# Kernel tuning notes

Measured on AMD Instinct MI355X. Metric: run time of the kernel, lower is better.

The kernel has to match this reference:

```python
import jax, jax.numpy as jnp
import numpy as np

EPS = 1.1920929e-07  # torch RMSNorm default eps = finfo(fp32).eps


def _rmsnorm(x, w):
    return x * jax.lax.rsqrt(jnp.mean(x * x, axis=-1, keepdims=True) + EPS) * w


def setup_inputs() -> dict:
    B, S, D, H, SD = 2, 2048, 1024, 16, 64
    ks = jax.random.split(jax.random.key(0), 16)
    scale = 0.02
    return {
        "x": jax.random.normal(ks[0], (B, S, D), jnp.float32),
        "gamma": jax.random.normal(ks[1], (1, 1, D), jnp.float32),
        "beta": jax.random.normal(ks[2], (1, 1, D), jnp.float32),
        "state": jax.random.normal(ks[3], (B, SD), jnp.float32),
        # weights stored as (in, out) so y = x @ W
        "w_qkv": jax.random.normal(ks[4], (D, 3 * D), jnp.float32) * scale,
        "w_o": jax.random.normal(ks[5], (D, D), jnp.float32) * scale,
        "w_gate": jax.random.normal(ks[6], (D, 3 * D), jnp.float32) * scale,
        "w_up": jax.random.normal(ks[7], (D, 3 * D), jnp.float32) * scale,
        "w_down": jax.random.normal(ks[8], (3 * D, D), jnp.float32) * scale,
        "norm1_w": jnp.ones((D,), jnp.float32),
        "norm2_w": jnp.ones((D,), jnp.float32),
        "w_state_mod": jax.random.normal(ks[9], (SD, 2 * D), jnp.float32) * scale,
        "w_h2s": jax.random.normal(ks[10], (D, SD), jnp.float32) * scale,
        "w_sgate": jax.random.normal(ks[11], (2 * SD, SD), jnp.float32) * scale,
    }


def reference(x, gamma, beta, state, w_qkv, w_o, w_gate, w_up, w_down,
              norm1_w, norm2_w, w_state_mod, w_h2s, w_sgate):
    B, S, D = x.shape
    H = 16
    hd = D // H

    # state-conditioned FiLM modulation
    state_mod = state @ w_state_mod                      # (B, 2D)
    state_gamma = 1.0 + state_mod[:, :D][:, None, :]     # (B, 1, D)
    state_beta = state_mod[:, D:][:, None, :]
    full_gamma = gamma * state_gamma
    full_beta = beta + state_beta

    # attention branch
    h = _rmsnorm(x, norm1_w) * full_gamma + full_beta
    qkv = (h @ w_qkv).reshape(B, S, 3, H, hd)
    q = qkv[:, :, 0].transpose(0, 2, 1, 3)               # (B, H, S, hd)
    k = qkv[:, :, 1].transpose(0, 2, 1, 3)
    v = qkv[:, :, 2].transpose(0, 2, 1, 3)
    scores = jnp.einsum('bhqd,bhkd->bhqk', q, k) / np.sqrt(hd).astype(np.float32)
    causal = jnp.tril(jnp.ones((S, S), bool))
    scores = jnp.where(causal, scores, -jnp.inf)
    attn = jax.nn.softmax(scores, axis=-1)
    out = jnp.einsum('bhqk,bhkd->bhqd', attn, v).transpose(0, 2, 1, 3).reshape(B, S, D)
    x = x + out @ w_o

    # SwiGLU FFN branch (same FiLM params)
    h2 = _rmsnorm(x, norm2_w) * full_gamma + full_beta
    gate = jax.nn.silu(h2 @ w_gate)
    x = x + (gate * (h2 @ w_up)) @ w_down

    # recurrent state update
    new_info = jnp.mean(x, axis=1) @ w_h2s               # (B, SD)
    update_gate = jax.nn.sigmoid(jnp.concatenate([state, new_info], axis=-1) @ w_sgate)
    new_state = state * (1.0 - update_gate) + new_info * update_gate
    return x, new_state
```

## Files before the change

kernel.cpp:

```cpp
#include <hip/hip_runtime.h>
#include <hip/hip_bf16.h>

#define EPS_RMS 1.1920929e-07f

constexpr int B_ = 2, S_ = 2048, D_ = 1024, H_ = 16, HD_ = 64, SD_ = 64;
constexpr int M_ = B_ * S_;
constexpr int D3_ = 3 * D_;

using short8 = __attribute__((ext_vector_type(8))) short;
using f32x4  = __attribute__((ext_vector_type(4))) float;
using f32x16 = __attribute__((ext_vector_type(16))) float;

static __device__ __forceinline__ ushort f2bf(float x) {
  __hip_bfloat16 h = __float2bfloat16(x);
  return *reinterpret_cast<ushort*>(&h);
}
static __device__ __forceinline__ float bf2f(ushort u) {
  __hip_bfloat16 h;
  *reinterpret_cast<ushort*>(&h) = u;
  return __bfloat162float(h);
}
static __device__ __forceinline__ unsigned pk2(float lo, float hi) {
  return (unsigned)f2bf(lo) | ((unsigned)f2bf(hi) << 16);
}
struct alignas(8) bf4 { ushort a, b, c, d; };

static __device__ __forceinline__ void gload16(const ushort* g, ushort* l) {
  __builtin_amdgcn_global_load_lds(
      (const __attribute__((address_space(1))) unsigned int*)g,
      (__attribute__((address_space(3))) unsigned int*)l, 16, 0, 0);
}

__global__ void film_kernel(const float* __restrict__ state,
                            const float* __restrict__ w_sm,
                            const float* __restrict__ gamma,
                            const float* __restrict__ beta,
                            float* __restrict__ fg, float* __restrict__ fb) {
  int c = blockIdx.x * 256 + threadIdx.x;
  int b = blockIdx.y;
  float acc = 0.f;
#pragma unroll 8
  for (int k = 0; k < SD_; ++k)
    acc += state[b * SD_ + k] * w_sm[k * (2 * D_) + c];
  if (c < D_) fg[b * D_ + c] = gamma[c] * (1.f + acc);
  else        fb[b * D_ + (c - D_)] = beta[c - D_] + acc;
}

__global__ __launch_bounds__(256) void rmsnorm_film_kernel(
    const float* __restrict__ X, const float* __restrict__ nw,
    const float* __restrict__ fg, const float* __restrict__ fb,
    ushort* __restrict__ Hout) {
  int row = blockIdx.x;
  int b = row / S_;
  int t = threadIdx.x;
  const float4* x4 = (const float4*)(X + (size_t)row * D_);
  float4 xv = x4[t];
  float ss = xv.x * xv.x + xv.y * xv.y + xv.z * xv.z + xv.w * xv.w;
#pragma unroll
  for (int off = 32; off >= 1; off >>= 1) ss += __shfl_xor(ss, off);
  __shared__ float red[4];
  if ((t & 63) == 0) red[t >> 6] = ss;
  __syncthreads();
  float tot = red[0] + red[1] + red[2] + red[3];
  float scale = rsqrtf(tot / (float)D_ + EPS_RMS);
  int d = t * 4;
  const float4 nw4 = *(const float4*)(nw + d);
  const float4 g4  = *(const float4*)(fg + b * D_ + d);
  const float4 b4  = *(const float4*)(fb + b * D_ + d);
  bf4 hv;
  hv.a = f2bf(xv.x * scale * nw4.x * g4.x + b4.x);
  hv.b = f2bf(xv.y * scale * nw4.y * g4.y + b4.y);
  hv.c = f2bf(xv.z * scale * nw4.z * g4.z + b4.z);
  hv.d = f2bf(xv.w * scale * nw4.w * g4.w + b4.w);
  *(bf4*)(Hout + (size_t)row * D_ + d) = hv;
}

__global__ __launch_bounds__(256) void transpose_bf16(
    const float* __restrict__ W, ushort* __restrict__ Wt, int K, int N) {
  __shared__ float tile[32][33];
  int n0 = blockIdx.x * 32, k0 = blockIdx.y * 32;
  int t = threadIdx.x;
  int c = t & 31, r = t >> 5;
#pragma unroll
  for (int p = 0; p < 4; ++p)
    tile[r + 8 * p][c] = W[(size_t)(k0 + r + 8 * p) * N + n0 + c];
  __syncthreads();
#pragma unroll
  for (int p = 0; p < 4; ++p)
    Wt[(size_t)(n0 + r + 8 * p) * K + k0 + c] = f2bf(tile[c][r + 8 * p]);
}

static __device__ __forceinline__ void mfma_tile(
    const char* Au, const char* Bu, f32x4 (&acc)[4][4],
    int l15, int l4, int swz, int wr, int wc) {
#pragma unroll
  for (int kk = 0; kk < 2; ++kk) {
    int tslot = ((kk * 4 + l4) ^ swz) << 4;
    short8 a[4], b[4];
#pragma unroll
    for (int i = 0; i < 4; ++i) {
      int arow = wr * 64 + i * 16 + l15;
      int brow = wc * 64 + i * 16 + l15;
      a[i] = *(const short8*)(Au + arow * 128 + tslot);
      b[i] = *(const short8*)(Bu + brow * 128 + tslot);
    }
#pragma unroll
    for (int m = 0; m < 4; ++m)
#pragma unroll
      for (int n = 0; n < 4; ++n)
        acc[m][n] = __builtin_amdgcn_mfma_f32_16x16x32_bf16(a[m], b[n], acc[m][n], 0, 0, 0);
  }
}

template<int EPI>
__global__ __launch_bounds__(256, 3) void gemm_mfma(
    const ushort* __restrict__ A, const ushort* __restrict__ Bt,
    const float* __restrict__ Res, const ushort* __restrict__ Gate,
    float* __restrict__ Cf, ushort* __restrict__ Cb, ushort* __restrict__ VtP,
    int M, int N, int K) {
  __shared__ ushort smem[16384];
  char* Au = (char*)smem;
  char* Bu = (char*)(smem + 8192);
  int t = threadIdx.x;

  int nbn = N >> 7;
  int nb  = nbn * (M >> 7);
  int qx  = nb >> 3;
  int lin = (blockIdx.x & 7) * qx + (blockIdx.x >> 3);
  int grp = lin / (nbn << 3), rem = lin % (nbn << 3);
  int bm = ((grp << 3) + (rem & 7)) << 7;
  int bn = (rem >> 3) << 7;

  int lane = t & 63, wid = t >> 6;
  int wr = wid >> 1, wc = wid & 1;
  int l15 = lane & 15, l4 = lane >> 4;
  int swz = l15 & 7;

  const ushort* gA[4];
  const ushort* gB[4];
  ushort* lA[4];
  ushort* lB[4];
#pragma unroll
  for (int p = 0; p < 4; ++p) {
    int seg = p * 4 + wid;
    int flat = seg * 64 + lane;
    int row = flat >> 3, sl = flat & 7;
    int gc = ((sl ^ (row & 7)) << 3);
    gA[p] = A  + (size_t)(bm + row) * K + gc;
    gB[p] = Bt + (size_t)(bn + row) * K + gc;
    lA[p] = smem + seg * 512;
    lB[p] = smem + 8192 + seg * 512;
  }

  f32x4 acc[4][4];
#pragma unroll
  for (int m = 0; m < 4; ++m)
#pragma unroll
    for (int n = 0; n < 4; ++n) acc[m][n] = (f32x4){0.f, 0.f, 0.f, 0.f};

  int nk = K >> 6;
  for (int kt = 0; kt < nk; ++kt) {
    __syncthreads();
#pragma unroll
    for (int p = 0; p < 4; ++p) {
      gload16(gA[p], lA[p]);
      gload16(gB[p], lB[p]);
      gA[p] += 64; gB[p] += 64;
    }
    __syncthreads();
    mfma_tile(Au, Bu, acc, l15, l4, swz, wr, wc);
  }

  if constexpr (EPI == 3) {
#pragma unroll
    for (int m = 0; m < 4; ++m)
#pragma unroll
      for (int n = 0; n < 4; ++n) {
        int row0 = bm + wr * 64 + m * 16 + l4 * 4;
        int col  = bn + wc * 64 + n * 16 + l15;
#pragma unroll
        for (int j = 0; j < 4; ++j) {
          size_t idx = (size_t)(row0 + j) * (size_t)N + col;
          Cf[idx] = Res[idx] + acc[m][n][j];
        }
      }
  } else {
    __syncthreads();
    ushort* Es = smem;
    bool vblk = (EPI == 4) && (bn >= 2048);
#pragma unroll
    for (int m = 0; m < 4; ++m)
#pragma unroll
      for (int n = 0; n < 4; ++n) {
        int rb0 = wr * 64 + m * 16 + l4 * 4;
        int c   = wc * 64 + n * 16 + l15;
#pragma unroll
        for (int j = 0; j < 4; ++j) {
          float v = acc[m][n][j];
          if constexpr (EPI == 1) v = v / (1.f + __expf(-v));
          int r = rb0 + j;
          if (vblk) Es[c * 128 + (r ^ ((c & 15) << 3))] = f2bf(v);
          else      Es[r * 128 + c] = f2bf(v);
        }
      }
    __syncthreads();
    if (vblk) {
#pragma unroll
      for (int p = 0; p < 8; ++p) {
        int flat = p * 256 + t;
        int c = flat >> 4, r8 = (flat & 15) * 8;
        int vc = bn - 2048 + c, hh = vc >> 6, dd = vc & 63;
        int bbv = bm >> 11, s0 = (bm & 2047) + r8;
        *(short8*)(VtP + ((((size_t)bbv * 16 + hh) * 64 + dd) << 11) + s0) =
            *(const short8*)&Es[c * 128 + (r8 ^ ((c & 15) << 3))];
      }
    } else {
#pragma unroll
      for (int p = 0; p < 8; ++p) {
        int flat = p * 256 + t;
        int r = flat >> 4, c8 = (flat & 15) * 8;
        size_t gidx = (size_t)(bm + r) * N + bn + c8;
        short8 es = *(const short8*)&Es[r * 128 + c8];
        if constexpr (EPI == 2) {
          union { short8 s; ushort u[8]; } a, b, o;
          a.s = es;
          b.s = *(const short8*)(Gate + gidx);
#pragma unroll
          for (int q = 0; q < 8; ++q) o.u[q] = f2bf(bf2f(a.u[q]) * bf2f(b.u[q]));
          *(short8*)(Cb + gidx) = o.s;
        } else {
          *(short8*)(Cb + gidx) = es;
        }
      }
    }
  }
}

__global__ __launch_bounds__(256, 2) void attn_mfma_kernel(
    const ushort* __restrict__ qkv,
    const ushort* __restrict__ Vt,
    ushort* __restrict__ AO) {
  __shared__ ushort lds[8192];
  const float SL2 = 0.125f * 1.44269504f;
  int t = threadIdx.x;
  int x = blockIdx.x;
  int lin = ((x & 7) << 6) + (x >> 3);
  int qtc = lin & 15;
  int hb  = lin >> 4;
  int h = hb & 15, bb = hb >> 4;
  int qt = qtc < 8 ? qtc : 23 - qtc;
  int q0 = qt * 128;
  int lane = t & 63, wv = t >> 6;
  int l31 = lane & 31, g = lane >> 5;

  const ushort* qrow_ptr = qkv + (size_t)(bb * S_ + q0 + wv * 32 + l31) * 3072 + h * 64;
  short8 qf[4];
#pragma unroll
  for (int s = 0; s < 4; ++s) qf[s] = *(const short8*)(qrow_ptr + s * 16 + g * 8);

  f32x16 accO[2];
#pragma unroll
  for (int u = 0; u < 2; ++u)
#pragma unroll
    for (int r = 0; r < 16; ++r) accO[u][r] = 0.f;
  float m = -INFINITY, l = 0.f;
  int qg = q0 + wv * 32 + l31;
  int qmin = q0 + wv * 32, qmax = qmin + 31;
  int ntiles = (q0 + 128) >> 6;

  const ushort* kbase = qkv + (size_t)(bb * S_) * 3072 + 1024 + h * 64;
  const ushort* vbase = Vt + ((size_t)(bb * 16 + h) * 64) * 2048;

  for (int kti = 0; kti < ntiles; ++kti) {
    int kt = kti << 6;
    __syncthreads();
#pragma unroll
    for (int p = 0; p < 2; ++p) {
      int flat = p * 256 + t;
      int row = flat >> 3, slot = flat & 7;
      *(short8*)&lds[row * 64 + ((slot ^ (row & 7)) << 3)] =
          *(const short8*)(kbase + (size_t)(kt + row) * 3072 + slot * 8);
      *(short8*)&lds[4096 + row * 64 + ((slot ^ (row & 7)) << 3)] =
          *(const short8*)(vbase + (size_t)row * 2048 + kt + slot * 8);
    }
    __syncthreads();
    if (kt > qmax) continue;

    f32x16 accT[2];
#pragma unroll
    for (int t2 = 0; t2 < 2; ++t2)
#pragma unroll
      for (int r = 0; r < 16; ++r) accT[t2][r] = 0.f;
#pragma unroll
    for (int t2 = 0; t2 < 2; ++t2) {
      int key = 32 * t2 + l31;
#pragma unroll
      for (int s = 0; s < 4; ++s) {
        short8 kf = *(const short8*)&lds[key * 64 + (((2 * s + g) ^ (key & 7)) << 3)];
        accT[t2] = __builtin_amdgcn_mfma_f32_32x32x16_bf16(kf, qf[s], accT[t2], 0, 0, 0);
      }
    }

    bool need_mask = (kt + 63 > qmin);
    float p_[2][16];
    float pmax = -INFINITY;
#pragma unroll
    for (int t2 = 0; t2 < 2; ++t2)
#pragma unroll
      for (int r = 0; r < 16; ++r) {
        float v = accT[t2][r] * SL2;
        if (need_mask) {
          int key = kt + 32 * t2 + (r & 3) + 8 * (r >> 2) + 4 * g;
          if (key > qg) v = -INFINITY;
        }
        p_[t2][r] = v;
        pmax = fmaxf(pmax, v);
      }
    pmax = fmaxf(pmax, __shfl_xor(pmax, 32));

    if (__any(pmax > m + 11.5f)) {
      float mnew = fmaxf(m, pmax);
      float corr = exp2f(m - mnew);
      m = mnew;
      l *= corr;
      float cr[16];
#pragma unroll
      for (int r = 0; r < 16; ++r) cr[r] = __shfl(corr, (r & 3) + 8 * (r >> 2) + 4 * g);
#pragma unroll
      for (int r = 0; r < 16; ++r) { accO[0][r] *= cr[r]; accO[1][r] *= cr[r]; }
    }
    float psum = 0.f;
#pragma unroll
    for (int t2 = 0; t2 < 2; ++t2)
#pragma unroll
      for (int r = 0; r < 16; ++r) {
        float e = exp2f(p_[t2][r] - m);
        p_[t2][r] = e;
        psum += e;
      }
    psum += __shfl_xor(psum, 32);
    l += psum;

#pragma unroll
    for (int s = 0; s < 4; ++s) {
      int ca = 2 * s, cb2 = 2 * s + 1;
      int ta = ca >> 2, ra = (ca & 3) * 4;
      int tb = cb2 >> 2, rbq = (cb2 & 3) * 4;
      unsigned w0a = pk2(p_[ta][ra], p_[ta][ra + 1]);
      unsigned w1a = pk2(p_[ta][ra + 2], p_[ta][ra + 3]);
      unsigned w0b = pk2(p_[tb][rbq], p_[tb][rbq + 1]);
      unsigned w1b = pk2(p_[tb][rbq + 2], p_[tb][rbq + 3]);
      unsigned x0a = __shfl_xor(w0a, 32), x1a = __shfl_xor(w1a, 32);
      unsigned x0b = __shfl_xor(w0b, 32), x1b = __shfl_xor(w1b, 32);
      union { unsigned u[4]; short8 s8; } pa;
      pa.u[0] = g ? x0b : w0a;
      pa.u[1] = g ? x1b : w1a;
      pa.u[2] = g ? w0b : x0a;
      pa.u[3] = g ? w1b : x1a;
#pragma unroll
      for (int u = 0; u < 2; ++u) {
        int d = 32 * u + l31;
        short8 vf = *(const short8*)&lds[4096 + d * 64 + (((2 * s + g) ^ (d & 7)) << 3)];
        accO[u] = __builtin_amdgcn_mfma_f32_32x32x16_bf16(pa.s8, vf, accO[u], 0, 0, 0);
      }
    }
  }

  float linv = 1.f / l;
  float lr[16];
#pragma unroll
  for (int r = 0; r < 16; ++r) lr[r] = __shfl(linv, (r & 3) + 8 * (r >> 2) + 4 * g);
  __syncthreads();
#pragma unroll
  for (int r = 0; r < 16; ++r) {
    int row = wv * 32 + (r & 3) + 8 * (r >> 2) + 4 * g;
    lds[row * 64 + l31]      = f2bf(accO[0][r] * lr[r]);
    lds[row * 64 + 32 + l31] = f2bf(accO[1][r] * lr[r]);
  }
  __syncthreads();
#pragma unroll
  for (int p = 0; p < 4; ++p) {
    int flat = p * 256 + t;
    int row = flat >> 3, slot = flat & 7;
    *(short8*)(AO + (size_t)(bb * S_ + q0 + row) * 1024 + h * 64 + slot * 8) =
        *(const short8*)&lds[row * 64 + slot * 8];
  }
}

__global__ void colmean1(const float* __restrict__ X, float* __restrict__ part) {
  int d = blockIdx.x * 256 + threadIdx.x;
  int b = blockIdx.y;
  int ch = blockIdx.z;
  float s = 0.f;
  int s0 = ch * (S_ / 16);
  for (int i = 0; i < S_ / 16; ++i)
    s += X[(size_t)(b * S_ + s0 + i) * D_ + d];
  part[(b * 16 + ch) * D_ + d] = s;
}
__global__ void colmean2(const float* __restrict__ part, float* __restrict__ cm) {
  int d = blockIdx.x * 256 + threadIdx.x;
  int b = blockIdx.y;
  float s = 0.f;
#pragma unroll
  for (int c = 0; c < 16; ++c) s += part[(b * 16 + c) * D_ + d];
  cm[b * D_ + d] = s * (1.f / (float)S_);
}

__global__ __launch_bounds__(128) void state_kernel(
    const float* __restrict__ cm, const float* __restrict__ state,
    const float* __restrict__ w_h2s, const float* __restrict__ w_sg,
    float* __restrict__ out_tail) {
  int t = threadIdx.x;
  int b = t >> 6, j = t & 63;
  float ni = 0.f;
  for (int k = 0; k < D_; ++k) ni += cm[b * D_ + k] * w_h2s[k * SD_ + j];
  __shared__ float ni_s[128];
  ni_s[t] = ni;
  __syncthreads();
  float g = 0.f;
#pragma unroll
  for (int k = 0; k < SD_; ++k) g += state[b * SD_ + k] * w_sg[k * SD_ + j];
#pragma unroll
  for (int k = 0; k < SD_; ++k) g += ni_s[b * SD_ + k] * w_sg[(SD_ + k) * SD_ + j];
  g = 1.f / (1.f + __expf(-g));
  float st = state[b * SD_ + j];
  out_tail[b * SD_ + j] = st * (1.f - g) + ni * g;
}

extern "C" void kernel_launch(void* const* d_in, const int* in_sizes, int n_in,
                              void* d_out, int out_size, void* d_ws, size_t ws_size,
                              hipStream_t stream) {
  const float* x      = (const float*)d_in[0];
  const float* gamma  = (const float*)d_in[1];
  const float* beta   = (const float*)d_in[2];
  const float* state  = (const float*)d_in[3];
  const float* w_qkv  = (const float*)d_in[4];
  const float* w_o    = (const float*)d_in[5];
  const float* w_gate = (const float*)d_in[6];
  const float* w_up   = (const float*)d_in[7];
  const float* w_down = (const float*)d_in[8];
  const float* norm1w = (const float*)d_in[9];
  const float* norm2w = (const float*)d_in[10];
  const float* w_sm   = (const float*)d_in[11];
  const float* w_h2s  = (const float*)d_in[12];
  const float* w_sg   = (const float*)d_in[13];
  float* out = (float*)d_out;

  float* ws = (float*)d_ws;
  float*  fg     = ws;
  float*  fb     = ws + 2048;
  float*  cm     = ws + 4096;
  float*  part   = ws + 8192;
  ushort* h_bf   = (ushort*)(ws + 65536);
  ushort* AO_bf  = (ushort*)(ws + 65536 + 2097152);
  ushort* wT     = (ushort*)(ws + 65536 + 2 * 2097152);
  ushort* qkv_bf = (ushort*)(ws + 65536 + 2 * 2097152 + 1572864);
  ushort* Vt_g   = (ushort*)(ws + 65536 + 2 * 2097152 + 1572864 + 6291456);
  ushort* gate_bf = qkv_bf;

  film_kernel<<<dim3(8, B_), 256, 0, stream>>>(state, w_sm, gamma, beta, fg, fb);
  rmsnorm_film_kernel<<<M_, 256, 0, stream>>>(x, norm1w, fg, fb, h_bf);
  transpose_bf16<<<dim3(D3_ / 32, D_ / 32), 256, 0, stream>>>(w_qkv, wT, D_, D3_);
  gemm_mfma<4><<<(D3_ / 128) * (M_ / 128), 256, 0, stream>>>(
      h_bf, wT, nullptr, nullptr, nullptr, qkv_bf, Vt_g, M_, D3_, D_);
  attn_mfma_kernel<<<512, 256, 0, stream>>>(qkv_bf, Vt_g, AO_bf);
  transpose_bf16<<<dim3(D_ / 32, D_ / 32), 256, 0, stream>>>(w_o, wT, D_, D_);
  gemm_mfma<3><<<(D_ / 128) * (M_ / 128), 256, 0, stream>>>(
      AO_bf, wT, x, nullptr, out, nullptr, nullptr, M_, D_, D_);
  rmsnorm_film_kernel<<<M_, 256, 0, stream>>>(out, norm2w, fg, fb, h_bf);
  transpose_bf16<<<dim3(D3_ / 32, D_ / 32), 256, 0, stream>>>(w_gate, wT, D_, D3_);
  gemm_mfma<1><<<(D3_ / 128) * (M_ / 128), 256, 0, stream>>>(
      h_bf, wT, nullptr, nullptr, nullptr, gate_bf, nullptr, M_, D3_, D_);
  transpose_bf16<<<dim3(D3_ / 32, D_ / 32), 256, 0, stream>>>(w_up, wT, D_, D3_);
  gemm_mfma<2><<<(D3_ / 128) * (M_ / 128), 256, 0, stream>>>(
      h_bf, wT, nullptr, gate_bf, nullptr, gate_bf, nullptr, M_, D3_, D_);
  transpose_bf16<<<dim3(D_ / 32, D3_ / 32), 256, 0, stream>>>(w_down, wT, D3_, D_);
  gemm_mfma<3><<<(D_ / 128) * (M_ / 128), 256, 0, stream>>>(
      gate_bf, wT, out, nullptr, out, nullptr, nullptr, M_, D_, D3_);
  colmean1<<<dim3(4, B_, 16), 256, 0, stream>>>(out, part);
  colmean2<<<dim3(4, B_), 256, 0, stream>>>(part, cm);
  state_kernel<<<1, 128, 0, stream>>>(cm, state, w_h2s, w_sg, out + (size_t)M_ * D_);
}
```

Measured before the change: 360.2 us.

## Fuse gate/up GEMMs into dual GEMM and pipeline paired-tile attention

The separate gate and up GEMMs become one dual-accumulator kernel. It reads the A tile once and applies SiLU(gate)*up in the epilogue, which removes a full GEMM's A traffic, the bf16 round trip of the gate intermediate, and one launch. The attention kernel now uses 512-thread blocks that pair a short and a long causal query tile to balance work. It double-buffers K/V in LDS with register prefetch and raises MFMA priority. The cost is a higher register count in the dual GEMM (launch bounds drop to 2 blocks) and twice the LDS in attention.

```diff
diff --git a/kernel.cpp b/kernel.cpp
--- a/kernel.cpp
+++ b/kernel.cpp
@@ -112,24 +112,29 @@
   }
 }
 
+static __device__ __forceinline__ void block_swizzle(int bid, int M, int N,
+                                                     int& bm, int& bn) {
+  int nbn = N >> 7;
+  int nb  = nbn * (M >> 7);
+  int qx  = nb >> 3;
+  int lin = (bid & 7) * qx + (bid >> 3);
+  int grp = lin / (nbn << 3), rem = lin % (nbn << 3);
+  bm = ((grp << 3) + (rem & 7)) << 7;
+  bn = (rem >> 3) << 7;
+}
+
 template<int EPI>
 __global__ __launch_bounds__(256, 3) void gemm_mfma(
     const ushort* __restrict__ A, const ushort* __restrict__ Bt,
-    const float* __restrict__ Res, const ushort* __restrict__ Gate,
+    const float* __restrict__ Res,
     float* __restrict__ Cf, ushort* __restrict__ Cb, ushort* __restrict__ VtP,
     int M, int N, int K) {
   __shared__ ushort smem[16384];
   char* Au = (char*)smem;
   char* Bu = (char*)(smem + 8192);
   int t = threadIdx.x;
-
-  int nbn = N >> 7;
-  int nb  = nbn * (M >> 7);
-  int qx  = nb >> 3;
-  int lin = (blockIdx.x & 7) * qx + (blockIdx.x >> 3);
-  int grp = lin / (nbn << 3), rem = lin % (nbn << 3);
-  int bm = ((grp << 3) + (rem & 7)) << 7;
-  int bn = (rem >> 3) << 7;
+  int bm, bn;
+  block_swizzle(blockIdx.x, M, N, bm, bn);
 
   int lane = t & 63, wid = t >> 6;
   int wr = wid >> 1, wc = wid & 1;
@@ -187,7 +192,7 @@
   } else {
     __syncthreads();
     ushort* Es = smem;
-    bool vblk = (EPI == 4) && (bn >= 2048);
+    bool vblk = (bn >= 2048);
 #pragma unroll
     for (int m = 0; m < 4; ++m)
 #pragma unroll
@@ -197,7 +202,6 @@
 #pragma unroll
         for (int j = 0; j < 4; ++j) {
           float v = acc[m][n][j];
-          if constexpr (EPI == 1) v = v / (1.f + __expf(-v));
           int r = rb0 + j;
           if (vblk) Es[c * 128 + (r ^ ((c & 15) << 3))] = f2bf(v);
           else      Es[r * 128 + c] = f2bf(v);
@@ -219,41 +223,131 @@
       for (int p = 0; p < 8; ++p) {
         int flat = p * 256 + t;
         int r = flat >> 4, c8 = (flat & 15) * 8;
-        size_t gidx = (size_t)(bm + r) * N + bn + c8;
-        short8 es = *(const short8*)&Es[r * 128 + c8];
-        if constexpr (EPI == 2) {
-          union { short8 s; ushort u[8]; } a, b, o;
-          a.s = es;
-          b.s = *(const short8*)(Gate + gidx);
-#pragma unroll
-          for (int q = 0; q < 8; ++q) o.u[q] = f2bf(bf2f(a.u[q]) * bf2f(b.u[q]));
-          *(short8*)(Cb + gidx) = o.s;
-        } else {
-          *(short8*)(Cb + gidx) = es;
-        }
-      }
-    }
-  }
-}
-
-__global__ __launch_bounds__(256, 2) void attn_mfma_kernel(
+        *(short8*)(Cb + (size_t)(bm + r) * N + bn + c8) = *(const short8*)&Es[r * 128 + c8];
+      }
+    }
+  }
+}
+
+__global__ __launch_bounds__(256, 2) void gemm_dual(
+    const ushort* __restrict__ A, const ushort* __restrict__ Gt,
+    const ushort* __restrict__ Ut, ushort* __restrict__ Cb,
+    int M, int N, int K) {
+  __shared__ ushort smem[24576];
+  char* Au = (char*)smem;
+  char* Gu = (char*)(smem + 8192);
+  char* Uu = (char*)(smem + 16384);
+  int t = threadIdx.x;
+  int bm, bn;
+  block_swizzle(blockIdx.x, M, N, bm, bn);
+
+  int lane = t & 63, wid = t >> 6;
+  int wr = wid >> 1, wc = wid & 1;
+  int l15 = lane & 15, l4 = lane >> 4;
+  int swz = l15 & 7;
+
+  const ushort* gA[4]; const ushort* gG[4]; const ushort* gU[4];
+  ushort* lA[4]; ushort* lG[4]; ushort* lU[4];
+#pragma unroll
+  for (int p = 0; p < 4; ++p) {
+    int seg = p * 4 + wid;
+    int flat = seg * 64 + lane;
+    int row = flat >> 3, sl = flat & 7;
+    int gc = ((sl ^ (row & 7)) << 3);
+    gA[p] = A  + (size_t)(bm + row) * K + gc;
+    gG[p] = Gt + (size_t)(bn + row) * K + gc;
+    gU[p] = Ut + (size_t)(bn + row) * K + gc;
+    lA[p] = smem + seg * 512;
+    lG[p] = smem + 8192 + seg * 512;
+    lU[p] = smem + 16384 + seg * 512;
+  }
+
+  f32x4 ag[4][4], au[4][4];
+#pragma unroll
+  for (int m = 0; m < 4; ++m)
+#pragma unroll
+    for (int n = 0; n < 4; ++n) {
+      ag[m][n] = (f32x4){0.f, 0.f, 0.f, 0.f};
+      au[m][n] = (f32x4){0.f, 0.f, 0.f, 0.f};
+    }
+
+  int nk = K >> 6;
+  for (int kt = 0; kt < nk; ++kt) {
+    __syncthreads();
+#pragma unroll
+    for (int p = 0; p < 4; ++p) {
+      gload16(gA[p], lA[p]);
+      gload16(gG[p], lG[p]);
+      gload16(gU[p], lU[p]);
+      gA[p] += 64; gG[p] += 64; gU[p] += 64;
+    }
+    __syncthreads();
+#pragma unroll
+    for (int kk = 0; kk < 2; ++kk) {
+      int tslot = ((kk * 4 + l4) ^ swz) << 4;
+      short8 a[4], bg[4], bu[4];
+#pragma unroll
+      for (int i = 0; i < 4; ++i) {
+        int arow = wr * 64 + i * 16 + l15;
+        int brow = wc * 64 + i * 16 + l15;
+        a[i]  = *(const short8*)(Au + arow * 128 + tslot);
+        bg[i] = *(const short8*)(Gu + brow * 128 + tslot);
+        bu[i] = *(const short8*)(Uu + brow * 128 + tslot);
+      }
+#pragma unroll
+      for (int m = 0; m < 4; ++m)
+#pragma unroll
+        for (int n = 0; n < 4; ++n) {
+          ag[m][n] = __builtin_amdgcn_mfma_f32_16x16x32_bf16(a[m], bg[n], ag[m][n], 0, 0, 0);
+          au[m][n] = __builtin_amdgcn_mfma_f32_16x16x32_bf16(a[m], bu[n], au[m][n], 0, 0, 0);
+        }
+    }
+  }
+
+  __syncthreads();
+  ushort* Es = smem;
+#pragma unroll
+  for (int m = 0; m < 4; ++m)
+#pragma unroll
+    for (int n = 0; n < 4; ++n) {
+      int rb0 = wr * 64 + m * 16 + l4 * 4;
+      int c   = wc * 64 + n * 16 + l15;
+#pragma unroll
+      for (int j = 0; j < 4; ++j) {
+        float gv = ag[m][n][j];
+        float v = gv / (1.f + __expf(-gv)) * au[m][n][j];
+        Es[(rb0 + j) * 128 + c] = f2bf(v);
+      }
+    }
+  __syncthreads();
+#pragma unroll
+  for (int p = 0; p < 8; ++p) {
+    int flat = p * 256 + t;
+    int r = flat >> 4, c8 = (flat & 15) * 8;
+    *(short8*)(Cb + (size_t)(bm + r) * N + bn + c8) = *(const short8*)&Es[r * 128 + c8];
+  }
+}
+
+__global__ __launch_bounds__(512, 2) void attn_mfma_kernel(
     const ushort* __restrict__ qkv,
     const ushort* __restrict__ Vt,
     ushort* __restrict__ AO) {
-  __shared__ ushort lds[8192];
+  __shared__ ushort lds[16384];
   const float SL2 = 0.125f * 1.44269504f;
   int t = threadIdx.x;
   int x = blockIdx.x;
-  int lin = ((x & 7) << 6) + (x >> 3);
-  int qtc = lin & 15;
-  int hb  = lin >> 4;
+  int lin = ((x & 7) << 5) + (x >> 3);
+  int pp = lin & 7;
+  int hb = lin >> 3;
   int h = hb & 15, bb = hb >> 4;
-  int qt = qtc < 8 ? qtc : 23 - qtc;
+  int lane = t & 63, wv = t >> 6;
+  int qi = wv >> 2, wsub = wv & 3;
+  int qt = qi ? (15 - pp) : pp;
   int q0 = qt * 128;
-  int lane = t & 63, wv = t >> 6;
   int l31 = lane & 31, g = lane >> 5;
 
-  const ushort* qrow_ptr = qkv + (size_t)(bb * S_ + q0 + wv * 32 + l31) * 3072 + h * 64;
+  int qrow = q0 + wsub * 32 + l31;
+  const ushort* qrow_ptr = qkv + (size_t)(bb * S_ + qrow) * 3072 + h * 64;
   short8 qf[4];
 #pragma unroll
   for (int s = 0; s < 4; ++s) qf[s] = *(const short8*)(qrow_ptr + s * 16 + g * 8);
@@ -264,113 +358,130 @@
 #pragma unroll
     for (int r = 0; r < 16; ++r) accO[u][r] = 0.f;
   float m = -INFINITY, l = 0.f;
-  int qg = q0 + wv * 32 + l31;
-  int qmin = q0 + wv * 32, qmax = qmin + 31;
-  int ntiles = (q0 + 128) >> 6;
+  int qg = qrow;
+  int qmin = q0 + wsub * 32, qmax = qmin + 31;
+  int nt = 2 * (16 - pp);
 
   const ushort* kbase = qkv + (size_t)(bb * S_) * 3072 + 1024 + h * 64;
   const ushort* vbase = Vt + ((size_t)(bb * 16 + h) * 64) * 2048;
 
-  for (int kti = 0; kti < ntiles; ++kti) {
+  int srow = t >> 3, sslot = t & 7;
+  int soff = srow * 64 + ((sslot ^ (srow & 7)) << 3);
+  const ushort* kg0 = kbase + (size_t)srow * 3072 + sslot * 8;
+  const ushort* vg0 = vbase + (size_t)srow * 2048 + sslot * 8;
+
+  *(short8*)&lds[soff] = *(const short8*)kg0;
+  *(short8*)&lds[4096 + soff] = *(const short8*)vg0;
+  __syncthreads();
+
+  for (int kti = 0; kti < nt; ++kti) {
+    int cur = kti & 1;
     int kt = kti << 6;
-    __syncthreads();
-#pragma unroll
-    for (int p = 0; p < 2; ++p) {
-      int flat = p * 256 + t;
-      int row = flat >> 3, slot = flat & 7;
-      *(short8*)&lds[row * 64 + ((slot ^ (row & 7)) << 3)] =
-          *(const short8*)(kbase + (size_t)(kt + row) * 3072 + slot * 8);
-      *(short8*)&lds[4096 + row * 64 + ((slot ^ (row & 7)) << 3)] =
-          *(const short8*)(vbase + (size_t)row * 2048 + kt + slot * 8);
-    }
-    __syncthreads();
-    if (kt > qmax) continue;
-
-    f32x16 accT[2];
-#pragma unroll
-    for (int t2 = 0; t2 < 2; ++t2)
-#pragma unroll
-      for (int r = 0; r < 16; ++r) accT[t2][r] = 0.f;
-#pragma unroll
-    for (int t2 = 0; t2 < 2; ++t2) {
-      int key = 32 * t2 + l31;
+    bool pf = (kti + 1 < nt);
+    short8 rk, rv;
+    if (pf) {
+      rk = *(const short8*)(kg0 + (size_t)(kti + 1) * (64 * 3072));
+      rv = *(const short8*)(vg0 + (kti + 1) * 64);
+    }
+    if (kt <= qmax) {
+      const ushort* Kb = lds + cur * 8192;
+      const ushort* Vb = Kb + 4096;
+
+      f32x16 accT[2];
+#pragma unroll
+      for (int t2 = 0; t2 < 2; ++t2)
+#pragma unroll
+        for (int r = 0; r < 16; ++r) accT[t2][r] = 0.f;
+      __builtin_amdgcn_s_setprio(1);
+#pragma unroll
+      for (int t2 = 0; t2 < 2; ++t2) {
+        int key = 32 * t2 + l31;
+#pragma unroll
+        for (int s = 0; s < 4; ++s) {
+          short8 kf = *(const short8*)&Kb[key * 64 + (((2 * s + g) ^ (key & 7)) << 3)];
+          accT[t2] = __builtin_amdgcn_mfma_f32_32x32x16_bf16(kf, qf[s], accT[t2], 0, 0, 0);
+        }
+      }
+      __builtin_amdgcn_s_setprio(0);
+
+      bool need_mask = (kt + 63 > qmin);
+      float p_[2][16];
+      float pmax = -INFINITY;
+#pragma unroll
+      for (int t2 = 0; t2 < 2; ++t2)
+#pragma unroll
+        for (int r = 0; r < 16; ++r) {
+          float v = accT[t2][r] * SL2;
+          if (need_mask) {
+            int key = kt + 32 * t2 + (r & 3) + 8 * (r >> 2) + 4 * g;
+            if (key > qg) v = -INFINITY;
+          }
+          p_[t2][r] = v;
+          pmax = fmaxf(pmax, v);
+        }
+      pmax = fmaxf(pmax, __shfl_xor(pmax, 32));
+
+      if (__any(pmax > m + 11.5f)) {
+        float mnew = fmaxf(m, pmax);
+        float corr = exp2f(m - mnew);
+        m = mnew;
+        l *= corr;
+        float cr[16];
+#pragma unroll
+        for (int r = 0; r < 16; ++r) cr[r] = __shfl(corr, (r & 3) + 8 * (r >> 2) + 4 * g);
+#pragma unroll
+        for (int r = 0; r < 16; ++r) { accO[0][r] *= cr[r]; accO[1][r] *= cr[r]; }
+      }
+      float psum = 0.f;
+#pragma unroll
+      for (int t2 = 0; t2 < 2; ++t2)
+#pragma unroll
+        for (int r = 0; r < 16; ++r) {
+          float e = exp2f(p_[t2][r] - m);
+          p_[t2][r] = e;
+          psum += e;
+        }
+      psum += __shfl_xor(psum, 32);
+      l += psum;
+
 #pragma unroll
       for (int s = 0; s < 4; ++s) {
-        short8 kf = *(const short8*)&lds[key * 64 + (((2 * s + g) ^ (key & 7)) << 3)];
-        accT[t2] = __builtin_amdgcn_mfma_f32_32x32x16_bf16(kf, qf[s], accT[t2], 0, 0, 0);
-      }
-    }
-
-    bool need_mask = (kt + 63 > qmin);
-    float p_[2][16];
-    float pmax = -INFINITY;
-#pragma unroll
-    for (int t2 = 0; t2 < 2; ++t2)
-#pragma unroll
-      for (int r = 0; r < 16; ++r) {
-        float v = accT[t2][r] * SL2;
-        if (need_mask) {
-          int key = kt + 32 * t2 + (r & 3) + 8 * (r >> 2) + 4 * g;
-          if (key > qg) v = -INFINITY;
-        }
-        p_[t2][r] = v;
-        pmax = fmaxf(pmax, v);
-      }
-    pmax = fmaxf(pmax, __shfl_xor(pmax, 32));
-
-    if (__any(pmax > m + 11.5f)) {
-      float mnew = fmaxf(m, pmax);
-      float corr = exp2f(m - mnew);
-      m = mnew;
-      l *= corr;
-      float cr[16];
-#pragma unroll
-      for (int r = 0; r < 16; ++r) cr[r] = __shfl(corr, (r & 3) + 8 * (r >> 2) + 4 * g);
-#pragma unroll
-      for (int r = 0; r < 16; ++r) { accO[0][r] *= cr[r]; accO[1][r] *= cr[r]; }
-    }
-    float psum = 0.f;
-#pragma unroll
-    for (int t2 = 0; t2 < 2; ++t2)
-#pragma unroll
-      for (int r = 0; r < 16; ++r) {
-        float e = exp2f(p_[t2][r] - m);
-        p_[t2][r] = e;
-        psum += e;
-      }
-    psum += __shfl_xor(psum, 32);
-    l += psum;
-
-#pragma unroll
-    for (int s = 0; s < 4; ++s) {
-      int ca = 2 * s, cb2 = 2 * s + 1;
-      int ta = ca >> 2, ra = (ca & 3) * 4;
-      int tb = cb2 >> 2, rbq = (cb2 & 3) * 4;
-      unsigned w0a = pk2(p_[ta][ra], p_[ta][ra + 1]);
-      unsigned w1a = pk2(p_[ta][ra + 2], p_[ta][ra + 3]);
-      unsigned w0b = pk2(p_[tb][rbq], p_[tb][rbq + 1]);
-      unsigned w1b = pk2(p_[tb][rbq + 2], p_[tb][rbq + 3]);
-      unsigned x0a = __shfl_xor(w0a, 32), x1a = __shfl_xor(w1a, 32);
-      unsigned x0b = __shfl_xor(w0b, 32), x1b = __shfl_xor(w1b, 32);
-      union { unsigned u[4]; short8 s8; } pa;
-      pa.u[0] = g ? x0b : w0a;
-      pa.u[1] = g ? x1b : w1a;
-      pa.u[2] = g ? w0b : x0a;
-      pa.u[3] = g ? w1b : x1a;
-#pragma unroll
-      for (int u = 0; u < 2; ++u) {
-        int d = 32 * u + l31;
-        short8 vf = *(const short8*)&lds[4096 + d * 64 + (((2 * s + g) ^ (d & 7)) << 3)];
-        accO[u] = __builtin_amdgcn_mfma_f32_32x32x16_bf16(pa.s8, vf, accO[u], 0, 0, 0);
-      }
-    }
+        int ca = 2 * s, cb2 = 2 * s + 1;
+        int ta = ca >> 2, ra = (ca & 3) * 4;
+        int tb = cb2 >> 2, rbq = (cb2 & 3) * 4;
+        unsigned w0a = pk2(p_[ta][ra], p_[ta][ra + 1]);
+        unsigned w1a = pk2(p_[ta][ra + 2], p_[ta][ra + 3]);
+        unsigned w0b = pk2(p_[tb][rbq], p_[tb][rbq + 1]);
+        unsigned w1b = pk2(p_[tb][rbq + 2], p_[tb][rbq + 3]);
+        unsigned x0a = __shfl_xor(w0a, 32), x1a = __shfl_xor(w1a, 32);
+        unsigned x0b = __shfl_xor(w0b, 32), x1b = __shfl_xor(w1b, 32);
+        union { unsigned u[4]; short8 s8; } pa;
+        pa.u[0] = g ? x0b : w0a;
+        pa.u[1] = g ? x1b : w1a;
+        pa.u[2] = g ? w0b : x0a;
+        pa.u[3] = g ? w1b : x1a;
+        __builtin_amdgcn_s_setprio(1);
+#pragma unroll
+        for (int u = 0; u < 2; ++u) {
+          int d = 32 * u + l31;
+          short8 vf = *(const short8*)&Vb[d * 64 + (((2 * s + g) ^ (d & 7)) << 3)];
+          accO[u] = __builtin_amdgcn_mfma_f32_32x32x16_bf16(pa.s8, vf, accO[u], 0, 0, 0);
+        }
+        __builtin_amdgcn_s_setprio(0);
+      }
+    }
+    if (pf) {
+      ushort* dst = lds + (cur ^ 1) * 8192;
+      *(short8*)&dst[soff] = rk;
+      *(short8*)&dst[4096 + soff] = rv;
+    }
+    __syncthreads();
   }
 
   float linv = 1.f / l;
   float lr[16];
 #pragma unroll
   for (int r = 0; r < 16; ++r) lr[r] = __shfl(linv, (r & 3) + 8 * (r >> 2) + 4 * g);
-  __syncthreads();
 #pragma unroll
   for (int r = 0; r < 16; ++r) {
     int row = wv * 32 + (r & 3) + 8 * (r >> 2) + 4 * g;
@@ -380,9 +491,11 @@
   __syncthreads();
 #pragma unroll
   for (int p = 0; p < 4; ++p) {
-    int flat = p * 256 + t;
+    int flat = p * 512 + t;
     int row = flat >> 3, slot = flat & 7;
-    *(short8*)(AO + (size_t)(bb * S_ + q0 + row) * 1024 + h * 64 + slot * 8) =
+    int qto = (row < 128) ? pp : (15 - pp);
+    int grow = row & 127;
+    *(short8*)(AO + (size_t)(bb * S_ + qto * 128 + grow) * 1024 + h * 64 + slot * 8) =
         *(const short8*)&lds[row * 64 + slot * 8];
   }
 }
@@ -454,29 +567,28 @@
   ushort* h_bf   = (ushort*)(ws + 65536);
   ushort* AO_bf  = (ushort*)(ws + 65536 + 2097152);
   ushort* wT     = (ushort*)(ws + 65536 + 2 * 2097152);
-  ushort* qkv_bf = (ushort*)(ws + 65536 + 2 * 2097152 + 1572864);
-  ushort* Vt_g   = (ushort*)(ws + 65536 + 2 * 2097152 + 1572864 + 6291456);
-  ushort* gate_bf = qkv_bf;
+  ushort* wT2    = (ushort*)(ws + 65536 + 2 * 2097152 + 1572864);
+  ushort* qkv_bf = (ushort*)(ws + 65536 + 2 * 2097152 + 2 * 1572864);
+  ushort* Vt_g   = (ushort*)(ws + 65536 + 2 * 2097152 + 2 * 1572864 + 6291456);
+  ushort* gu_bf  = qkv_bf;
 
   film_kernel<<<dim3(8, B_), 256, 0, stream>>>(state, w_sm, gamma, beta, fg, fb);
   rmsnorm_film_kernel<<<M_, 256, 0, stream>>>(x, norm1w, fg, fb, h_bf);
   transpose_bf16<<<dim3(D3_ / 32, D_ / 32), 256, 0, stream>>>(w_qkv, wT, D_, D3_);
   gemm_mfma<4><<<(D3_ / 128) * (M_ / 128), 256, 0, stream>>>(
-      h_bf, wT, nullptr, nullptr, nullptr, qkv_bf, Vt_g, M_, D3_, D_);
-  attn_mfma_kernel<<<512, 256, 0, stream>>>(qkv_bf, Vt_g, AO_bf);
+      h_bf, wT, nullptr, nullptr, qkv_bf, Vt_g, M_, D3_, D_);
+  attn_mfma_kernel<<<256, 512, 0, stream>>>(qkv_bf, Vt_g, AO_bf);
   transpose_bf16<<<dim3(D_ / 32, D_ / 32), 256, 0, stream>>>(w_o, wT, D_, D_);
   gemm_mfma<3><<<(D_ / 128) * (M_ / 128), 256, 0, stream>>>(
-      AO_bf, wT, x, nullptr, out, nullptr, nullptr, M_, D_, D_);
+      AO_bf, wT, x, out, nullptr, nullptr, M_, D_, D_);
   rmsnorm_film_kernel<<<M_, 256, 0, stream>>>(out, norm2w, fg, fb, h_bf);
   transpose_bf16<<<dim3(D3_ / 32, D_ / 32), 256, 0, stream>>>(w_gate, wT, D_, D3_);
-  gemm_mfma<1><<<(D3_ / 128) * (M_ / 128), 256, 0, stream>>>(
-      h_bf, wT, nullptr, nullptr, nullptr, gate_bf, nullptr, M_, D3_, D_);
-  transpose_bf16<<<dim3(D3_ / 32, D_ / 32), 256, 0, stream>>>(w_up, wT, D_, D3_);
-  gemm_mfma<2><<<(D3_ / 128) * (M_ / 128), 256, 0, stream>>>(
-      h_bf, wT, nullptr, gate_bf, nullptr, gate_bf, nullptr, M_, D3_, D_);
+  transpose_bf16<<<dim3(D3_ / 32, D_ / 32), 256, 0, stream>>>(w_up, wT2, D_, D3_);
+  gemm_dual<<<(D3_ / 128) * (M_ / 128), 256, 0, stream>>>(
+      h_bf, wT, wT2, gu_bf, M_, D3_, D_);
   transpose_bf16<<<dim3(D_ / 32, D3_ / 32), 256, 0, stream>>>(w_down, wT, D3_, D_);
   gemm_mfma<3><<<(D_ / 128) * (M_ / 128), 256, 0, stream>>>(
-      gate_bf, wT, out, nullptr, out, nullptr, nullptr, M_, D_, D3_);
+      gu_bf, wT, out, out, nullptr, nullptr, M_, D_, D3_);
   colmean1<<<dim3(4, B_, 16), 256, 0, stream>>>(out, part);
   colmean2<<<dim3(4, B_), 256, 0, stream>>>(part, cm);
   state_kernel<<<1, 128, 0, stream>>>(cm, state, w_h2s, w_sg, out + (size_t)M_ * D_);
```

Measured after the change: 323.2 us. -10.3%, faster.
